# Kernel optimization log

Hardware: AMD Instinct MI355X
Metric: run time of the kernel (lower is better)

## Reference

```python
import jax, jax.numpy as jnp
import numpy as np

N_LOWF, N_HIGHF, E, D, L = 100000, 100000, 1600000, 32, 2
EPS = 1e-5
SLOPE = 0.2  # GATv2 default negative_slope


def _segment_softmax(e, seg, n):
    m = jax.ops.segment_max(e, seg, num_segments=n)
    m = jnp.where(jnp.isfinite(m), m, 0.0)
    ex = jnp.exp(e - m[seg])
    s = jax.ops.segment_sum(ex, seg, num_segments=n)
    return ex / (s[seg] + 1e-16)


def _gcn(x, src, dst, n, W, b):
    # GCNConv with add_self_loops=True, normalize=True (PyG defaults)
    h = x @ W  # [n, D]
    deg = jax.ops.segment_sum(jnp.ones(src.shape[0], x.dtype), dst, num_segments=n) + 1.0
    dinv = jax.lax.rsqrt(deg)
    msg = h[src] * (dinv[src] * dinv[dst])[:, None]  # [E, D]
    out = jax.ops.segment_sum(msg, dst, num_segments=n)
    out = out + h * (1.0 / deg)[:, None]  # self-loop term deg^-1
    return out + b


def _gatv2(x_src, x_dst, src, dst, n_dst, Wl, Wr, att, b):
    # GATv2Conv, heads=1, add_self_loops=False
    hl = x_src @ Wl  # [n_src, D]
    hr = x_dst @ Wr  # [n_dst, D]
    e = jax.nn.leaky_relu(hl[src] + hr[dst], SLOPE) @ att  # [E]
    alpha = _segment_softmax(e, dst, n_dst)
    out = jax.ops.segment_sum(hl[src] * alpha[:, None], dst, num_segments=n_dst)
    return out + b


def _bn(x, g, b):
    mu = jnp.mean(x, axis=0)
    var = jnp.mean(jnp.square(x - mu), axis=0)
    return g * (x - mu) * jax.lax.rsqrt(var + EPS) + b


def _forward(x_lowf, x_highf, gcn_ll_W, gcn_ll_b, gcn_hh_W, gcn_hh_b,
             gat_hl_Wl, gat_hl_Wr, gat_hl_att, gat_hl_b,
             gat_lh_Wl, gat_lh_Wr, gat_lh_att, gat_lh_b,
             bn_lowf_gamma, bn_lowf_beta, bn_highf_gamma, bn_highf_beta,
             ei_ll, ei_hh, ei_hl, ei_lh):
    xl, xh = x_lowf, x_highf
    for i in range(L):
        # HeteroConv with aggr='sum' over relations targeting each node type
        new_l = (_gcn(xl, ei_ll[0], ei_ll[1], N_LOWF, gcn_ll_W[i], gcn_ll_b[i])
                 + _gatv2(xh, xl, ei_hl[0], ei_hl[1], N_LOWF,
                          gat_hl_Wl[i], gat_hl_Wr[i], gat_hl_att[i], gat_hl_b[i]))
        new_h = (_gcn(xh, ei_hh[0], ei_hh[1], N_HIGHF, gcn_hh_W[i], gcn_hh_b[i])
                 + _gatv2(xl, xh, ei_lh[0], ei_lh[1], N_HIGHF,
                          gat_lh_Wl[i], gat_lh_Wr[i], gat_lh_att[i], gat_lh_b[i]))
        # per-node-type BatchNorm + ReLU (dropout = identity in eval)
        xl = jax.nn.relu(_bn(new_l, bn_lowf_gamma[i], bn_lowf_beta[i]))
        xh = jax.nn.relu(_bn(new_h, bn_highf_gamma[i], bn_highf_beta[i]))
    return jnp.concatenate([xl, xh], axis=0)  # [N_LOWF+N_HIGHF, D]


def setup_inputs() -> dict:
    key = jax.random.key(0)
    ks = jax.random.split(key, 32)
    rn = lambda i, s: jax.random.normal(ks[i], s, dtype=jnp.float32) * 0.1
    ri = lambda i, n: jax.random.randint(ks[i], (2, E), 0, n, dtype=jnp.int64)
    return {
        "x_lowf": rn(0, (N_LOWF, D)),
        "x_highf": rn(1, (N_HIGHF, D)),
        "gcn_ll_W": rn(2, (L, D, D)), "gcn_ll_b": jnp.zeros((L, D), jnp.float32),
        "gcn_hh_W": rn(3, (L, D, D)), "gcn_hh_b": jnp.zeros((L, D), jnp.float32),
        "gat_hl_Wl": rn(4, (L, D, D)), "gat_hl_Wr": rn(5, (L, D, D)),
        "gat_hl_att": rn(6, (L, D)), "gat_hl_b": jnp.zeros((L, D), jnp.float32),
        "gat_lh_Wl": rn(7, (L, D, D)), "gat_lh_Wr": rn(8, (L, D, D)),
        "gat_lh_att": rn(9, (L, D)), "gat_lh_b": jnp.zeros((L, D), jnp.float32),
        "bn_lowf_gamma": jnp.ones((L, D), jnp.float32), "bn_lowf_beta": jnp.zeros((L, D), jnp.float32),
        "bn_highf_gamma": jnp.ones((L, D), jnp.float32), "bn_highf_beta": jnp.zeros((L, D), jnp.float32),
        "ei_ll": ri(10, N_LOWF),
        "ei_hh": ri(11, N_HIGHF),
        "ei_hl": jnp.stack([jax.random.randint(ks[12], (E,), 0, N_HIGHF, dtype=jnp.int64),
                            jax.random.randint(ks[13], (E,), 0, N_LOWF, dtype=jnp.int64)]),
        "ei_lh": jnp.stack([jax.random.randint(ks[14], (E,), 0, N_LOWF, dtype=jnp.int64),
                            jax.random.randint(ks[15], (E,), 0, N_HIGHF, dtype=jnp.int64)]),
    }


def reference(x_lowf, x_highf, gcn_ll_W, gcn_ll_b, gcn_hh_W, gcn_hh_b,
              gat_hl_Wl, gat_hl_Wr, gat_hl_att, gat_hl_b,
              gat_lh_Wl, gat_lh_Wr, gat_lh_att, gat_lh_b,
              bn_lowf_gamma, bn_lowf_beta, bn_highf_gamma, bn_highf_beta,
              ei_ll, ei_hh, ei_hl, ei_lh):
    return _forward(x_lowf, x_highf, gcn_ll_W, gcn_ll_b, gcn_hh_W, gcn_hh_b,
                    gat_hl_Wl, gat_hl_Wr, gat_hl_att, gat_hl_b,
                    gat_lh_Wl, gat_lh_Wr, gat_lh_att, gat_lh_b,
                    bn_lowf_gamma, bn_lowf_beta, bn_highf_gamma, bn_highf_beta,
                    ei_ll, ei_hh, ei_hl, ei_lh)
```

## Files before the change

### kernel.cpp

```cpp
#include <hip/hip_runtime.h>
#include <hip/hip_fp16.h>

#define NN 100000
#define EDG 1600000
#define LAY 2
#define NBKT 98
#define BKTPAD 128
#define CAP 18432
#define PCHUNK 2560
#define CPR 625

static inline int cdiv(int a, int b) { return (a + b - 1) / b; }

__global__ void k_init(int* bhist, float* stats) {
    int t = blockIdx.x * blockDim.x + threadIdx.x;
    if (t < 4 * BKTPAD) bhist[t] = 0;
    if (t < 4 * 64) stats[t] = 0.f;
}

__global__ __launch_bounds__(256) void k_bhist(const int* __restrict__ ll,
                                               const int* __restrict__ hh,
                                               const int* __restrict__ hl,
                                               const int* __restrict__ lh, int* __restrict__ bhist) {
    __shared__ int h[NBKT];
    int tid = threadIdx.x;
    if (tid < NBKT) h[tid] = 0;
    __syncthreads();
    int r = blockIdx.x / CPR;
    int chunk = blockIdx.x - r * CPR;
    const int* dst = (r == 0 ? ll : r == 1 ? hh : r == 2 ? hl : lh) + EDG;
    int base = chunk * PCHUNK;
#pragma unroll
    for (int k = 0; k < 10; k++) {
        int d = dst[base + k * 256 + tid];
        atomicAdd(&h[d >> 10], 1);
    }
    __syncthreads();
    if (tid < NBKT) atomicAdd(&bhist[r * BKTPAD + tid], h[tid]);
}

__global__ void k_bscan(const int* __restrict__ bhist, int* __restrict__ bases,
                        int* __restrict__ gcursor, int* __restrict__ rp) {
    __shared__ int sh[BKTPAD];
    int t = threadIdx.x;
    for (int r = 0; r < 4; r++) {
        int v = (t < BKTPAD) ? ((t < NBKT) ? bhist[r * BKTPAD + t] : 0) : 0;
        if (t < BKTPAD) sh[t] = v;
        __syncthreads();
        for (int off = 1; off < BKTPAD; off <<= 1) {
            int x = (t < BKTPAD && t >= off) ? sh[t - off] : 0;
            __syncthreads();
            if (t < BKTPAD) sh[t] += x;
            __syncthreads();
        }
        if (t < BKTPAD) {
            int ex = sh[t] - v;
            bases[r * BKTPAD + t] = ex;
            gcursor[r * BKTPAD + t] = ex;
        }
        __syncthreads();
    }
    if (t < 4) rp[t * (NN + 1) + NN] = EDG;
}

__global__ __launch_bounds__(256) void k_partition(const int* __restrict__ ll,
                                                   const int* __restrict__ hh,
                                                   const int* __restrict__ hl,
                                                   const int* __restrict__ lh,
                                                   int* __restrict__ gcursor,
                                                   int2* __restrict__ pairs) {
    __shared__ int lhist[NBKT], lbase[NBKT];
    int tid = threadIdx.x;
    if (tid < NBKT) lhist[tid] = 0;
    __syncthreads();
    int r = blockIdx.x / CPR;
    int chunk = blockIdx.x - r * CPR;
    const int* ei = (r == 0 ? ll : r == 1 ? hh : r == 2 ? hl : lh);
    const int* srcp = ei;
    const int* dstp = ei + EDG;
    int base = chunk * PCHUNK;
    int s[10], d[10], rk[10];
#pragma unroll
    for (int k = 0; k < 10; k++) {
        int e = base + k * 256 + tid;
        s[k] = srcp[e];
        d[k] = dstp[e];
        rk[k] = atomicAdd(&lhist[d[k] >> 10], 1);
    }
    __syncthreads();
    if (tid < NBKT) lbase[tid] = atomicAdd(&gcursor[r * BKTPAD + tid], lhist[tid]);
    __syncthreads();
    int2* pr = pairs + (size_t)r * EDG;
#pragma unroll
    for (int k = 0; k < 10; k++) {
        int b = d[k] >> 10;
        pr[lbase[b] + rk[k]] = make_int2(s[k], d[k]);
    }
}

__global__ __launch_bounds__(256) void k_build(const int2* __restrict__ pairs,
                                               const int* __restrict__ bases,
                                               const int* __restrict__ bhist, int* __restrict__ rp,
                                               int* __restrict__ cs) {
    __shared__ int cnt_arr[1024];
    __shared__ int sh[256];
    __shared__ int srcs[CAP];
    int tid = threadIdx.x;
    int r = blockIdx.x / NBKT;
    int b = blockIdx.x - r * NBKT;
    int base = bases[r * BKTPAD + b];
    int cnt = bhist[r * BKTPAD + b];
    int d0 = b << 10;
    int ndst = NN - d0;
    if (ndst > 1024) ndst = 1024;
#pragma unroll
    for (int j = 0; j < 4; j++) cnt_arr[4 * tid + j] = 0;
    __syncthreads();
    const int2* pr = pairs + (size_t)r * EDG + base;
    for (int i = tid; i < cnt; i += 256) {
        int2 p = pr[i];
        atomicAdd(&cnt_arr[p.y - d0], 1);
    }
    __syncthreads();
    int c0 = cnt_arr[4 * tid], c1 = cnt_arr[4 * tid + 1], c2 = cnt_arr[4 * tid + 2],
        c3 = cnt_arr[4 * tid + 3];
    int s = c0 + c1 + c2 + c3;
    sh[tid] = s;
    __syncthreads();
    for (int off = 1; off < 256; off <<= 1) {
        int x = (tid >= off) ? sh[tid - off] : 0;
        __syncthreads();
        sh[tid] += x;
        __syncthreads();
    }
    int run = sh[tid] - s;
    int st0 = run, st1 = st0 + c0, st2 = st1 + c1, st3 = st2 + c2;
    cnt_arr[4 * tid] = st0;
    cnt_arr[4 * tid + 1] = st1;
    cnt_arr[4 * tid + 2] = st2;
    cnt_arr[4 * tid + 3] = st3;
    int* rpr = rp + r * (NN + 1);
    if (4 * tid + 0 < ndst) rpr[d0 + 4 * tid + 0] = base + st0;
    if (4 * tid + 1 < ndst) rpr[d0 + 4 * tid + 1] = base + st1;
    if (4 * tid + 2 < ndst) rpr[d0 + 4 * tid + 2] = base + st2;
    if (4 * tid + 3 < ndst) rpr[d0 + 4 * tid + 3] = base + st3;
    __syncthreads();
    for (int i = tid; i < cnt; i += 256) {
        int2 p = pr[i];
        int pos = atomicAdd(&cnt_arr[p.y - d0], 1);
        if (pos < CAP) srcs[pos] = p.x;
    }
    __syncthreads();
    int* csr = cs + (size_t)r * EDG + base;
    for (int i = tid; i < cnt; i += 256) csr[i] = (i < CAP) ? srcs[i] : 0;
}

__global__ void k_dinv(const int* __restrict__ rp, float* __restrict__ dinv_l,
                       float* __restrict__ dinv_h) {
    int i = blockIdx.x * blockDim.x + threadIdx.x;
    if (i >= 2 * NN) return;
    int r = (i < NN) ? 0 : 1, j = (i < NN) ? i : i - NN;
    const int* rpr = rp + r * (NN + 1);
    float deg = (float)(rpr[j + 1] - rpr[j]) + 1.f;
    float v = rsqrtf(deg);
    if (r == 0) dinv_l[j] = v;
    else dinv_h[j] = v;
}

__global__ __launch_bounds__(256) void k_gemm3(const float* __restrict__ x,
                                               const float* __restrict__ stats,
                                               const float* __restrict__ gamma,
                                               const float* __restrict__ beta,
                                               const float* __restrict__ W0,
                                               const float* __restrict__ W1,
                                               const float* __restrict__ W2,
                                               const float* __restrict__ scale0,
                                               __half* __restrict__ y0, __half* __restrict__ y1,
                                               __half* __restrict__ y2) {
    __shared__ float Ws[3][1024];
    __shared__ float xs[8][32];
    int tid = threadIdx.x;
    for (int i = tid; i < 1024; i += 256) {
        Ws[0][i] = W0[i];
        Ws[1][i] = W1[i];
        Ws[2][i] = W2[i];
    }
    int c = tid & 31, rl = tid >> 5;
    float mu = 0.f, gs = 1.f, be = 0.f;
    if (stats) {
        const float inv_n = 1.f / (float)NN;
        mu = stats[c] * inv_n;
        float var = stats[32 + c] * inv_n - mu * mu;
        gs = gamma[c] * rsqrtf(var + 1e-5f);
        be = beta[c];
    }
    for (int r0 = blockIdx.x * 8; r0 < NN; r0 += gridDim.x * 8) {
        int r = r0 + rl;
        __syncthreads();
        if (r < NN) {
            float xv = x[(size_t)r * 32 + c];
            if (stats) {
                xv = gs * (xv - mu) + be;
                xv = (xv > 0.f) ? xv : 0.f;
            }
            xs[rl][c] = xv;
        }
        __syncthreads();
        if (r < NN) {
            float a0 = 0.f, a1 = 0.f, a2 = 0.f;
#pragma unroll
            for (int k = 0; k < 32; k++) {
                float xv = xs[rl][k];
                a0 += xv * Ws[0][k * 32 + c];
                a1 += xv * Ws[1][k * 32 + c];
                a2 += xv * Ws[2][k * 32 + c];
            }
            a0 *= scale0[r];
            y0[(size_t)r * 32 + c] = __float2half(a0);
            y1[(size_t)r * 32 + c] = __float2half(a1);
            y2[(size_t)r * 32 + c] = __float2half(a2);
        }
    }
}

__device__ inline void cvt8(int4 r, float2* f) {
    const __half2* h = (const __half2*)&r;
    f[0] = __half22float2(h[0]);
    f[1] = __half22float2(h[1]);
    f[2] = __half22float2(h[2]);
    f[3] = __half22float2(h[3]);
}

__global__ __launch_bounds__(256) void k_aggregate(
    const int* __restrict__ rp_gcn, const int* __restrict__ cs_gcn,
    const __half* __restrict__ h_gcn, const float* __restrict__ dinv,
    const int* __restrict__ rp_gat, const int* __restrict__ cs_gat,
    const __half* __restrict__ h_gl, const __half* __restrict__ h_gr,
    const float* __restrict__ attv, const float* __restrict__ b_gcn,
    const float* __restrict__ b_gat, float* __restrict__ out, float* __restrict__ stats) {
    int tid = threadIdx.x;
    int c4 = tid & 3;
    int g = tid >> 2;
    int v = blockIdx.x * 64 + g;
    bool alive = v < NN;

    const int4* hg4 = (const int4*)h_gcn;
    const int4* hl4 = (const int4*)h_gl;
    const int4* hr4p = (const int4*)h_gr;
    const float2* at2 = (const float2*)attv;

    float2 a[4];
#pragma unroll
    for (int q = 0; q < 4; q++) a[q] = at2[c4 * 4 + q];

    float2 res[4];
#pragma unroll
    for (int q = 0; q < 4; q++) res[q] = make_float2(0.f, 0.f);

    if (alive) {
        const int4 zero4 = make_int4(0, 0, 0, 0);
        float2 acc[4];
#pragma unroll
        for (int q = 0; q < 4; q++) acc[q] = make_float2(0.f, 0.f);
        int b0 = rp_gcn[v], e0 = rp_gcn[v + 1];
        for (int e = b0; e < e0; e += 4) {
            int myi = cs_gcn[min(e + c4, e0 - 1)];
            int4 raw[4];
#pragma unroll
            for (int j = 0; j < 4; j++) {
                int sj = __shfl(myi, j, 4);
                raw[j] = ((e + j) < e0) ? hg4[(size_t)sj * 4 + c4] : zero4;
            }
#pragma unroll
            for (int j = 0; j < 4; j++) {
                float2 f[4];
                cvt8(raw[j], f);
#pragma unroll
                for (int q = 0; q < 4; q++) {
                    acc[q].x += f[q].x;
                    acc[q].y += f[q].y;
                }
            }
        }
        {
            int4 selfr = hg4[(size_t)v * 4 + c4];
            float2 f[4];
            cvt8(selfr, f);
#pragma unroll
            for (int q = 0; q < 4; q++) {
                acc[q].x += f[q].x;
                acc[q].y += f[q].y;
            }
        }
        float dv = dinv[v];
        float2 hr[4];
        {
            int4 rr = hr4p[(size_t)v * 4 + c4];
            cvt8(rr, hr);
        }
        float m = -3.0e38f, ss = 0.f;
        float2 o[4];
#pragma unroll
        for (int q = 0; q < 4; q++) o[q] = make_float2(0.f, 0.f);
        int b1 = rp_gat[v], e1 = rp_gat[v + 1];
        for (int e = b1; e < e1; e += 4) {
            int myi = cs_gat[min(e + c4, e1 - 1)];
            int4 raw[4];
#pragma unroll
            for (int j = 0; j < 4; j++) {
                int sj = __shfl(myi, j, 4);
                raw[j] = hl4[(size_t)sj * 4 + c4];
            }
            float p[4];
#pragma unroll
            for (int j = 0; j < 4; j++) {
                float2 f[4];
                cvt8(raw[j], f);
                float pj = 0.f;
#pragma unroll
                for (int q = 0; q < 4; q++) {
                    float tx = f[q].x + hr[q].x;
                    tx = (tx > 0.f) ? tx : 0.2f * tx;
                    float ty = f[q].y + hr[q].y;
                    ty = (ty > 0.f) ? ty : 0.2f * ty;
                    pj += tx * a[q].x + ty * a[q].y;
                }
                p[j] = pj;
            }
#pragma unroll
            for (int off = 1; off <= 2; off <<= 1) {
#pragma unroll
                for (int j = 0; j < 4; j++) p[j] += __shfl_xor(p[j], off, 4);
            }
#pragma unroll
            for (int j = 0; j < 4; j++)
                if ((e + j) >= e1) p[j] = -3.0e38f;
            float cmax = fmaxf(fmaxf(p[0], p[1]), fmaxf(p[2], p[3]));
            float mn = fmaxf(m, cmax);
            float sc = __expf(m - mn);
            float wsum = 0.f;
            float2 oa[4];
#pragma unroll
            for (int q = 0; q < 4; q++) oa[q] = make_float2(0.f, 0.f);
#pragma unroll
            for (int j = 0; j < 4; j++) {
                float w = __expf(p[j] - mn);
                wsum += w;
                float2 f[4];
                cvt8(raw[j], f);
#pragma unroll
                for (int q = 0; q < 4; q++) {
                    oa[q].x += w * f[q].x;
                    oa[q].y += w * f[q].y;
                }
            }
            ss = ss * sc + wsum;
#pragma unroll
            for (int q = 0; q < 4; q++) {
                o[q].x = o[q].x * sc + oa[q].x;
                o[q].y = o[q].y * sc + oa[q].y;
            }
            m = mn;
        }
        float inv = 1.f / (ss + 1e-16f);
#pragma unroll
        for (int q = 0; q < 4; q++) {
            float bx = b_gcn[c4 * 8 + 2 * q] + b_gat[c4 * 8 + 2 * q];
            float by = b_gcn[c4 * 8 + 2 * q + 1] + b_gat[c4 * 8 + 2 * q + 1];
            res[q].x = acc[q].x * dv + o[q].x * inv + bx;
            res[q].y = acc[q].y * dv + o[q].y * inv + by;
        }
        float4* o4 = (float4*)(out + (size_t)v * 32 + c4 * 8);
        o4[0] = make_float4(res[0].x, res[0].y, res[1].x, res[1].y);
        o4[1] = make_float4(res[2].x, res[2].y, res[3].x, res[3].y);
    }
    float s1[8], s2[8];
#pragma unroll
    for (int q = 0; q < 4; q++) {
        s1[2 * q] = res[q].x;
        s1[2 * q + 1] = res[q].y;
        s2[2 * q] = res[q].x * res[q].x;
        s2[2 * q + 1] = res[q].y * res[q].y;
    }
#pragma unroll
    for (int off = 4; off <= 32; off <<= 1) {
#pragma unroll
        for (int k = 0; k < 8; k++) {
            s1[k] += __shfl_xor(s1[k], off, 64);
            s2[k] += __shfl_xor(s2[k], off, 64);
        }
    }
    __shared__ float sst[4][2][32];
    int wave = tid >> 6, lane = tid & 63;
    if (lane < 4) {
#pragma unroll
        for (int k = 0; k < 8; k++) {
            sst[wave][0][lane * 8 + k] = s1[k];
            sst[wave][1][lane * 8 + k] = s2[k];
        }
    }
    __syncthreads();
    if (tid < 64) {
        int which = tid >> 5, col = tid & 31;
        float t = sst[0][which][col] + sst[1][which][col] + sst[2][which][col] +
                  sst[3][which][col];
        atomicAdd(&stats[which * 32 + col], t);
    }
}

__global__ void k_bn_apply(const float* __restrict__ x, const float* __restrict__ stats,
                           const float* __restrict__ gamma, const float* __restrict__ beta,
                           float* __restrict__ y) {
    int total4 = NN * 8;
    const float inv_n = 1.f / (float)NN;
    const float4* x4 = (const float4*)x;
    float4* y4 = (float4*)y;
    for (int i = blockIdx.x * blockDim.x + threadIdx.x; i < total4; i += gridDim.x * blockDim.x) {
        int c0 = (i * 4) & 31;
        float4 v = x4[i];
        float r[4] = {v.x, v.y, v.z, v.w};
#pragma unroll
        for (int j = 0; j < 4; j++) {
            int c = c0 + j;
            float mu = stats[c] * inv_n;
            float var = stats[32 + c] * inv_n - mu * mu;
            float gs = gamma[c] * rsqrtf(var + 1e-5f);
            float t = gs * (r[j] - mu) + beta[c];
            r[j] = (t > 0.f) ? t : 0.f;
        }
        y4[i] = make_float4(r[0], r[1], r[2], r[3]);
    }
}

extern "C" void kernel_launch(void* const* d_in, const int* in_sizes, int n_in, void* d_out,
                              int out_size, void* d_ws, size_t ws_size, hipStream_t stream) {
    const float* x_l = (const float*)d_in[0];
    const float* x_h = (const float*)d_in[1];
    const float* Wll = (const float*)d_in[2];
    const float* bll = (const float*)d_in[3];
    const float* Whh = (const float*)d_in[4];
    const float* bhh = (const float*)d_in[5];
    const float* Whl_l = (const float*)d_in[6];
    const float* Whl_r = (const float*)d_in[7];
    const float* att_hl = (const float*)d_in[8];
    const float* b_hl = (const float*)d_in[9];
    const float* Wlh_l = (const float*)d_in[10];
    const float* Wlh_r = (const float*)d_in[11];
    const float* att_lh = (const float*)d_in[12];
    const float* b_lh = (const float*)d_in[13];
    const float* g_l = (const float*)d_in[14];
    const float* be_l = (const float*)d_in[15];
    const float* g_h = (const float*)d_in[16];
    const float* be_h = (const float*)d_in[17];
    const int* ei_ll = (const int*)d_in[18];
    const int* ei_hh = (const int*)d_in[19];
    const int* ei_hl = (const int*)d_in[20];
    const int* ei_lh = (const int*)d_in[21];

    char* p = (char*)d_ws;
    auto alloc = [&](size_t bytes) -> void* {
        void* r = (void*)p;
        p += (bytes + 255) & ~(size_t)255;
        return r;
    };
    const size_t HFEAT = (size_t)NN * 32 * sizeof(__half);
    const size_t FFEAT = (size_t)NN * 32 * sizeof(float);
    int2* pairs = (int2*)alloc((size_t)4 * EDG * sizeof(int2));
    float* new_l = (float*)pairs;
    float* new_h = (float*)((char*)pairs + FFEAT);
    __half* hgcn_l = (__half*)alloc(HFEAT);
    __half* hgcn_h = (__half*)alloc(HFEAT);
    __half* hgl_hl = (__half*)alloc(HFEAT);
    __half* hgr_hl = (__half*)alloc(HFEAT);
    __half* hgl_lh = (__half*)alloc(HFEAT);
    __half* hgr_lh = (__half*)alloc(HFEAT);
    int* cs = (int*)alloc((size_t)4 * EDG * sizeof(int));
    int* rp = (int*)alloc((size_t)4 * (NN + 1) * sizeof(int));
    float* dinv_l = (float*)alloc(NN * sizeof(float));
    float* dinv_h = (float*)alloc(NN * sizeof(float));
    int* bhist = (int*)alloc(4 * BKTPAD * sizeof(int));
    int* bases = (int*)alloc(4 * BKTPAD * sizeof(int));
    int* gcursor = (int*)alloc(4 * BKTPAD * sizeof(int));
    float* stats = (float*)alloc(4 * 64 * sizeof(float));

    const int TB = 256;
    k_init<<<2, TB, 0, stream>>>(bhist, stats);
    k_bhist<<<4 * CPR, TB, 0, stream>>>(ei_ll, ei_hh, ei_hl, ei_lh, bhist);
    k_bscan<<<1, TB, 0, stream>>>(bhist, bases, gcursor, rp);
    k_partition<<<4 * CPR, TB, 0, stream>>>(ei_ll, ei_hh, ei_hl, ei_lh, gcursor, pairs);
    k_build<<<4 * NBKT, TB, 0, stream>>>(pairs, bases, bhist, rp, cs);
    k_dinv<<<cdiv(2 * NN, TB), TB, 0, stream>>>(rp, dinv_l, dinv_h);

    const int* rp0 = rp;
    const int* rp1 = rp + (NN + 1);
    const int* rp2 = rp + 2 * (NN + 1);
    const int* rp3 = rp + 3 * (NN + 1);
    const int* cs0 = cs;
    const int* cs1 = cs + (size_t)EDG;
    const int* cs2 = cs + (size_t)2 * EDG;
    const int* cs3 = cs + (size_t)3 * EDG;

    const int GRID = 2048;
    const int AGRID = cdiv(NN, 64);
    float* st0l = stats;
    float* st0h = stats + 64;
    float* st1l = stats + 128;
    float* st1h = stats + 192;

    k_gemm3<<<GRID, TB, 0, stream>>>(x_l, nullptr, nullptr, nullptr, Wll, Whl_r, Wlh_l, dinv_l,
                                     hgcn_l, hgr_hl, hgl_lh);
    k_gemm3<<<GRID, TB, 0, stream>>>(x_h, nullptr, nullptr, nullptr, Whh, Wlh_r, Whl_l, dinv_h,
                                     hgcn_h, hgr_lh, hgl_hl);
    k_aggregate<<<AGRID, TB, 0, stream>>>(rp0, cs0, hgcn_l, dinv_l, rp2, cs2, hgl_hl, hgr_hl,
                                          att_hl, bll, b_hl, new_l, st0l);
    k_aggregate<<<AGRID, TB, 0, stream>>>(rp1, cs1, hgcn_h, dinv_h, rp3, cs3, hgl_lh, hgr_lh,
                                          att_lh, bhh, b_lh, new_h, st0h);
    k_gemm3<<<GRID, TB, 0, stream>>>(new_l, st0l, g_l, be_l, Wll + 1024, Whl_r + 1024,
                                     Wlh_l + 1024, dinv_l, hgcn_l, hgr_hl, hgl_lh);
    k_gemm3<<<GRID, TB, 0, stream>>>(new_h, st0h, g_h, be_h, Whh + 1024, Wlh_r + 1024,
                                     Whl_l + 1024, dinv_h, hgcn_h, hgr_lh, hgl_hl);
    k_aggregate<<<AGRID, TB, 0, stream>>>(rp0, cs0, hgcn_l, dinv_l, rp2, cs2, hgl_hl, hgr_hl,
                                          att_hl + 32, bll + 32, b_hl + 32, new_l, st1l);
    k_aggregate<<<AGRID, TB, 0, stream>>>(rp1, cs1, hgcn_h, dinv_h, rp3, cs3, hgl_lh, hgr_lh,
                                          att_lh + 32, bhh + 32, b_lh + 32, new_h, st1h);
    k_bn_apply<<<GRID, TB, 0, stream>>>(new_l, st1l, g_l + 32, be_l + 32, (float*)d_out);
    k_bn_apply<<<GRID, TB, 0, stream>>>(new_h, st1h, g_h + 32, be_h + 32,
                                        ((float*)d_out) + (size_t)NN * 32);
}
```

Measured before the change: 679.2 us.

## Pack edge pairs into 32-bit words and gather 8 neighbors per iteration

The partition step now stores each edge as one 32-bit word holding the local destination offset in the top 10 bits and the source id in the low 22 bits, replacing the 8-byte int2 pair. This halves the scatter writes in partition and the reads in the CSR build. The fused GCN/GATv2 aggregation loops now gather 8 neighbor rows per iteration instead of 4, putting more loads in flight per thread at the cost of more registers. The pairs buffer also backs the new_l/new_h aliases and is now half the size, so it must still be large enough for both.

```diff
diff --git a/kernel.cpp b/kernel.cpp
--- a/kernel.cpp
+++ b/kernel.cpp
@@ -68,7 +68,7 @@
                                                    const int* __restrict__ hl,
                                                    const int* __restrict__ lh,
                                                    int* __restrict__ gcursor,
-                                                   int2* __restrict__ pairs) {
+                                                   unsigned* __restrict__ pairs) {
     __shared__ int lhist[NBKT], lbase[NBKT];
     int tid = threadIdx.x;
     if (tid < NBKT) lhist[tid] = 0;
@@ -90,15 +90,16 @@
     __syncthreads();
     if (tid < NBKT) lbase[tid] = atomicAdd(&gcursor[r * BKTPAD + tid], lhist[tid]);
     __syncthreads();
-    int2* pr = pairs + (size_t)r * EDG;
+    unsigned* pr = pairs + (size_t)r * EDG;
 #pragma unroll
     for (int k = 0; k < 10; k++) {
         int b = d[k] >> 10;
-        pr[lbase[b] + rk[k]] = make_int2(s[k], d[k]);
-    }
-}
-
-__global__ __launch_bounds__(256) void k_build(const int2* __restrict__ pairs,
+        unsigned w = ((unsigned)(d[k] & 1023) << 22) | (unsigned)s[k];
+        pr[lbase[b] + rk[k]] = w;
+    }
+}
+
+__global__ __launch_bounds__(256) void k_build(const unsigned* __restrict__ pairs,
                                                const int* __restrict__ bases,
                                                const int* __restrict__ bhist, int* __restrict__ rp,
                                                int* __restrict__ cs) {
@@ -116,10 +117,10 @@
 #pragma unroll
     for (int j = 0; j < 4; j++) cnt_arr[4 * tid + j] = 0;
     __syncthreads();
-    const int2* pr = pairs + (size_t)r * EDG + base;
+    const unsigned* pr = pairs + (size_t)r * EDG + base;
     for (int i = tid; i < cnt; i += 256) {
-        int2 p = pr[i];
-        atomicAdd(&cnt_arr[p.y - d0], 1);
+        unsigned w = pr[i];
+        atomicAdd(&cnt_arr[w >> 22], 1);
     }
     __syncthreads();
     int c0 = cnt_arr[4 * tid], c1 = cnt_arr[4 * tid + 1], c2 = cnt_arr[4 * tid + 2],
@@ -146,9 +147,9 @@
     if (4 * tid + 3 < ndst) rpr[d0 + 4 * tid + 3] = base + st3;
     __syncthreads();
     for (int i = tid; i < cnt; i += 256) {
-        int2 p = pr[i];
-        int pos = atomicAdd(&cnt_arr[p.y - d0], 1);
-        if (pos < CAP) srcs[pos] = p.x;
+        unsigned w = pr[i];
+        int pos = atomicAdd(&cnt_arr[w >> 22], 1);
+        if (pos < CAP) srcs[pos] = (int)(w & 0x3FFFFFu);
     }
     __syncthreads();
     int* csr = cs + (size_t)r * EDG + base;
@@ -263,16 +264,22 @@
 #pragma unroll
         for (int q = 0; q < 4; q++) acc[q] = make_float2(0.f, 0.f);
         int b0 = rp_gcn[v], e0 = rp_gcn[v + 1];
-        for (int e = b0; e < e0; e += 4) {
-            int myi = cs_gcn[min(e + c4, e0 - 1)];
-            int4 raw[4];
+        for (int e = b0; e < e0; e += 8) {
+            int i0 = cs_gcn[min(e + c4, e0 - 1)];
+            int i1 = cs_gcn[min(e + 4 + c4, e0 - 1)];
+            int4 raw[8];
 #pragma unroll
             for (int j = 0; j < 4; j++) {
-                int sj = __shfl(myi, j, 4);
+                int sj = __shfl(i0, j, 4);
                 raw[j] = ((e + j) < e0) ? hg4[(size_t)sj * 4 + c4] : zero4;
             }
 #pragma unroll
             for (int j = 0; j < 4; j++) {
+                int sj = __shfl(i1, j, 4);
+                raw[4 + j] = ((e + 4 + j) < e0) ? hg4[(size_t)sj * 4 + c4] : zero4;
+            }
+#pragma unroll
+            for (int j = 0; j < 8; j++) {
                 float2 f[4];
                 cvt8(raw[j], f);
 #pragma unroll
@@ -303,17 +310,23 @@
 #pragma unroll
         for (int q = 0; q < 4; q++) o[q] = make_float2(0.f, 0.f);
         int b1 = rp_gat[v], e1 = rp_gat[v + 1];
-        for (int e = b1; e < e1; e += 4) {
-            int myi = cs_gat[min(e + c4, e1 - 1)];
-            int4 raw[4];
+        for (int e = b1; e < e1; e += 8) {
+            int i0 = cs_gat[min(e + c4, e1 - 1)];
+            int i1 = cs_gat[min(e + 4 + c4, e1 - 1)];
+            int4 raw[8];
 #pragma unroll
             for (int j = 0; j < 4; j++) {
-                int sj = __shfl(myi, j, 4);
+                int sj = __shfl(i0, j, 4);
                 raw[j] = hl4[(size_t)sj * 4 + c4];
             }
-            float p[4];
 #pragma unroll
             for (int j = 0; j < 4; j++) {
+                int sj = __shfl(i1, j, 4);
+                raw[4 + j] = hl4[(size_t)sj * 4 + c4];
+            }
+            float p[8];
+#pragma unroll
+            for (int j = 0; j < 8; j++) {
                 float2 f[4];
                 cvt8(raw[j], f);
                 float pj = 0.f;
@@ -330,12 +343,14 @@
 #pragma unroll
             for (int off = 1; off <= 2; off <<= 1) {
 #pragma unroll
-                for (int j = 0; j < 4; j++) p[j] += __shfl_xor(p[j], off, 4);
-            }
-#pragma unroll
-            for (int j = 0; j < 4; j++)
+                for (int j = 0; j < 8; j++) p[j] += __shfl_xor(p[j], off, 4);
+            }
+#pragma unroll
+            for (int j = 0; j < 8; j++)
                 if ((e + j) >= e1) p[j] = -3.0e38f;
-            float cmax = fmaxf(fmaxf(p[0], p[1]), fmaxf(p[2], p[3]));
+            float cmax = p[0];
+#pragma unroll
+            for (int j = 1; j < 8; j++) cmax = fmaxf(cmax, p[j]);
             float mn = fmaxf(m, cmax);
             float sc = __expf(m - mn);
             float wsum = 0.f;
@@ -343,7 +358,7 @@
 #pragma unroll
             for (int q = 0; q < 4; q++) oa[q] = make_float2(0.f, 0.f);
 #pragma unroll
-            for (int j = 0; j < 4; j++) {
+            for (int j = 0; j < 8; j++) {
                 float w = __expf(p[j] - mn);
                 wsum += w;
                 float2 f[4];
@@ -465,7 +480,7 @@
     };
     const size_t HFEAT = (size_t)NN * 32 * sizeof(__half);
     const size_t FFEAT = (size_t)NN * 32 * sizeof(float);
-    int2* pairs = (int2*)alloc((size_t)4 * EDG * sizeof(int2));
+    unsigned* pairs = (unsigned*)alloc((size_t)4 * EDG * sizeof(unsigned));
     float* new_l = (float*)pairs;
     float* new_h = (float*)((char*)pairs + FFEAT);
     __half* hgcn_l = (__half*)alloc(HFEAT);
```

Measured after the change: 695.4 us. +2.4%, slower.
